# Performance work log

Measured on AMD Instinct MI355X. Metric: run time of the kernel, lower is better.

## Reference

```python
import jax, jax.numpy as jnp
import numpy as np

N = 50000      # nodes
E = 600000     # edges (avg degree 12)
DIN, DE, DH = 17, 1, 128
L, H, C = 3, 4, 32   # layers, heads, per-head channels (DH = H*C)
NEG_SLOPE = 0.2


def setup_inputs() -> dict:
    key = jax.random.key(0)
    ks = jax.random.split(key, 18)
    rn = lambda k, s, sc: jax.random.normal(k, s, jnp.float32) * sc
    return {
        "x": rn(ks[0], (N, DIN), 1.0),
        "edge_index": jax.random.randint(ks[1], (2, E), 0, N, dtype=jnp.int64),
        "edge_attr": rn(ks[2], (E, DE), 1.0),
        "enc_node_w": rn(ks[3], (DIN, DH), 1.0 / np.sqrt(DIN)),
        "enc_node_b": jnp.zeros((DH,), jnp.float32),
        "enc_edge_w": rn(ks[4], (DE, DH), 1.0),
        "enc_edge_b": jnp.zeros((DH,), jnp.float32),
        "lin_w": rn(ks[5], (L, DH, DH), 1.0 / np.sqrt(DH)),
        "lin_edge_w": rn(ks[6], (L, DH, DH), 1.0 / np.sqrt(DH)),
        "att_src": rn(ks[7], (L, H, C), 1.0 / np.sqrt(C)),
        "att_dst": rn(ks[8], (L, H, C), 1.0 / np.sqrt(C)),
        "att_edge": rn(ks[9], (L, H, C), 1.0 / np.sqrt(C)),
        "gat_bias": jnp.zeros((L, DH), jnp.float32),
        "dec_w1": rn(ks[10], (DH, DH), 1.0 / np.sqrt(DH)),
        "dec_b1": jnp.zeros((DH,), jnp.float32),
        "dec_w2": rn(ks[11], (DH, 2), 1.0 / np.sqrt(DH)),
        "dec_b2": jnp.zeros((2,), jnp.float32),
    }


def _gat_layer(x, src, dst, e_attr, W, We, a_src, a_dst, a_edge, bias):
    """PyG GATConv, concat=True, dropout in eval mode (identity).
    x: [N,DH], src/dst: [E2] (self-loops already appended), e_attr: [E2,DH]."""
    n = x.shape[0]
    h = (x @ W).reshape(n, H, C)                       # [N,H,C]
    alpha_src = jnp.einsum('nhc,hc->nh', h, a_src)     # [N,H]
    alpha_dst = jnp.einsum('nhc,hc->nh', h, a_dst)
    e = (e_attr @ We).reshape(-1, H, C)                # [E2,H,C]
    alpha_e = jnp.einsum('ehc,hc->eh', e, a_edge)      # [E2,H]
    logits = jax.nn.leaky_relu(alpha_src[src] + alpha_dst[dst] + alpha_e, NEG_SLOPE)
    # segment softmax over edges grouped by destination node
    mx = jax.ops.segment_max(logits, dst, num_segments=n)          # [N,H]
    num = jnp.exp(logits - mx[dst])                                # [E2,H]
    den = jax.ops.segment_sum(num, dst, num_segments=n)            # [N,H]
    alpha = num / (den[dst] + 1e-16)                               # [E2,H]
    msg = h[src] * alpha[:, :, None]                               # [E2,H,C]
    out = jax.ops.segment_sum(msg, dst, num_segments=n)            # [N,H,C]
    return out.reshape(n, H * C) + bias


def reference(x, edge_index, edge_attr,
              enc_node_w, enc_node_b, enc_edge_w, enc_edge_b,
              lin_w, lin_edge_w, att_src, att_dst, att_edge, gat_bias,
              dec_w1, dec_b1, dec_w2, dec_b2):
    n = x.shape[0]
    src, dst = edge_index[0], edge_index[1]
    h = x @ enc_node_w + enc_node_b                    # node encoder
    ea = edge_attr @ enc_edge_w + enc_edge_b           # edge encoder [E,DH]
    # add_self_loops with fill_value='mean': self-loop attr = mean of incoming edge attrs
    ea_sum = jax.ops.segment_sum(ea, dst, num_segments=n)
    cnt = jax.ops.segment_sum(jnp.ones((ea.shape[0],), ea.dtype), dst, num_segments=n)
    loop_attr = ea_sum / jnp.maximum(cnt, 1.0)[:, None]
    loop_idx = jnp.arange(n, dtype=src.dtype)
    src_f = jnp.concatenate([src, loop_idx])
    dst_f = jnp.concatenate([dst, loop_idx])
    ea_f = jnp.concatenate([ea, loop_attr], axis=0)    # [E+N,DH]
    for l in range(L):
        h = _gat_layer(h, src_f, dst_f, ea_f,
                       lin_w[l], lin_edge_w[l],
                       att_src[l], att_dst[l], att_edge[l], gat_bias[l])
        h = jax.nn.elu(h)
    h = jax.nn.relu(h @ dec_w1 + dec_b1)
    return h @ dec_w2 + dec_b2                          # [N,2]
```

## Files before the change

kernel.cpp:

```cpp
#include <hip/hip_runtime.h>
#include <hip/hip_fp16.h>
#include <math.h>

#define DIN 17
#define DH  128
#define NH  4
#define CC  32
#define NL  3
#define NEG 0.2f

#define PK_SHIFT 44
#define PK_MASK  ((1ULL << PK_SHIFT) - 1)
#define PK_BIAS  16.0f
#define PK_SCALE 1048576.0f

typedef _Float16 hf;
typedef _Float16 f16x8 __attribute__((ext_vector_type(8)));
typedef float    f32x4 __attribute__((ext_vector_type(4)));

#define NT 9

__global__ void pq_kernel(const float* __restrict__ ew, const float* __restrict__ eb,
                          const float* __restrict__ We, const float* __restrict__ ae,
                          float* __restrict__ pq) {
    int lh = blockIdx.x;
    int l = lh >> 2, h = lh & 3;
    int t = threadIdx.x;
    const float* Wel = We + l * DH * DH;
    const float* ael = ae + l * DH + h * CC;
    float p = 0.f, q = 0.f;
    for (int d = t; d < DH; d += 64) {
        const float* row = Wel + d * DH + h * CC;
        float wp = 0.f;
        for (int c = 0; c < CC; ++c) wp += row[c] * ael[c];
        p += ew[d] * wp;
        q += eb[d] * wp;
    }
    for (int o = 32; o > 0; o >>= 1) { p += __shfl_down(p, o, 64); q += __shfl_down(q, o, 64); }
    if (t == 0) { pq[lh * 2 + 0] = p; pq[lh * 2 + 1] = q; }
}

__global__ void vprep(const float* __restrict__ lin_w, const float* __restrict__ att_src,
                      const float* __restrict__ att_dst, float* __restrict__ va) {
    int b = blockIdx.x;
    int l = b >> 3, id = b & 7, hh = id >> 1;
    const float* W = lin_w + (size_t)l * DH * DH;
    const float* a = ((id & 1) ? att_dst : att_src) + l * DH + hh * CC;
    int k = threadIdx.x;
    float s = 0.f;
    #pragma unroll
    for (int c = 0; c < CC; ++c) s += W[k * DH + hh * CC + c] * a[c];
    va[(size_t)b * DH + k] = s;
}

__global__ void wtprep(const float* __restrict__ lin_w, const float* __restrict__ dec_w1,
                       const float* __restrict__ va, hf* __restrict__ wfrag) {
    int b = blockIdx.x;
    int m = b / NT, nt = b % NT;
    int lane = threadIdx.x & 63, kk = threadIdx.x >> 6;
    int colr = lane & 15, kg = lane >> 4;
    hf* dst = wfrag + ((((size_t)b * 4 + kk) * 64) + lane) * 8;
    if (nt < 8) {
        const float* src = (m < 3) ? (lin_w + (size_t)m * DH * DH) : dec_w1;
        #pragma unroll
        for (int jj = 0; jj < 8; ++jj) {
            int k = kk * 32 + kg * 8 + jj;
            dst[jj] = (hf)src[k * DH + nt * 16 + colr];
        }
    } else {
        #pragma unroll
        for (int jj = 0; jj < 8; ++jj) {
            int k = kk * 32 + kg * 8 + jj;
            dst[jj] = (m < 3 && colr < 8) ? (hf)va[((size_t)m * 8 + colr) * DH + k] : (hf)0.f;
        }
    }
}

__global__ void enc_kernel(const float* __restrict__ x, const float* __restrict__ W,
                           const float* __restrict__ b, float* __restrict__ h, int N) {
    __shared__ float wl[DIN][DH];
    __shared__ float xs[32][DIN];
    int tid = threadIdx.x;
    int row0 = blockIdx.x * 32;
    for (int i = tid; i < DIN * DH; i += 256) wl[i / DH][i % DH] = W[i];
    for (int i = tid; i < 32 * DIN; i += 256) {
        int r = i / DIN, k = i % DIN;
        int rr = row0 + r; if (rr > N - 1) rr = N - 1;
        xs[r][k] = x[(size_t)rr * DIN + k];
    }
    __syncthreads();
    int c = tid & 127;
    int g = tid >> 7;
    float bias = b[c];
    #pragma unroll
    for (int r = 0; r < 16; ++r) {
        int row = row0 + g * 16 + r;
        if (row >= N) break;
        float acc = bias;
        #pragma unroll
        for (int k = 0; k < DIN; ++k) acc += xs[g * 16 + r][k] * wl[k][c];
        h[(size_t)row * DH + c] = acc;
    }
}

#define STAGE_ROWS(hsrc)                                                          \
    {                                                                             \
        _Pragma("unroll")                                                         \
        for (int i = 0; i < 4; ++i) {                                             \
            int idx = tid + i * 256;           \
            int r = idx >> 4, ch = idx & 15;                                      \
            int gr = row0 + r; if (gr > N - 1) gr = N - 1;                        \
            const float4* sp = (const float4*)((hsrc) + (size_t)gr * DH + ch * 8);\
            float4 v0 = sp[0], v1 = sp[1];                                        \
            union { uint4 u; hf hx[8]; } pkd;                                     \
            pkd.hx[0] = (hf)v0.x; pkd.hx[1] = (hf)v0.y;                           \
            pkd.hx[2] = (hf)v0.z; pkd.hx[3] = (hf)v0.w;                           \
            pkd.hx[4] = (hf)v1.x; pkd.hx[5] = (hf)v1.y;                           \
            pkd.hx[6] = (hf)v1.z; pkd.hx[7] = (hf)v1.w;                           \
            lds[r * 16 + (ch ^ (r & 7))] = pkd.u;                                 \
        }                                                                         \
        __syncthreads();                                                          \
    }

__global__ void __launch_bounds__(256) layer_node(
        const float* __restrict__ h, const hf* __restrict__ wfrag,
        __half* __restrict__ h1h, float* __restrict__ as_, float* __restrict__ ad_,
        int N) {
    __shared__ uint4 lds[64 * 16];
    int tid = threadIdx.x;
    int row0 = blockIdx.x * 64;
    STAGE_ROWS(h);

    int w = tid >> 6, lane = tid & 63;
    int colr = lane & 15, kg = lane >> 4;
    int lrow = w * 16 + colr;

    f16x8 afr[4];
    #pragma unroll
    for (int kk = 0; kk < 4; ++kk) {
        int ch = (kk * 4 + kg) ^ (colr & 7);
        afr[kk] = *(const f16x8*)&lds[lrow * 16 + ch];
    }

    f32x4 acc[NT];
    #pragma unroll
    for (int nt = 0; nt < NT; ++nt) acc[nt] = (f32x4){0.f, 0.f, 0.f, 0.f};

    const f16x8* wf = (const f16x8*)wfrag;
    #pragma unroll
    for (int nt = 0; nt < NT; ++nt) {
        #pragma unroll
        for (int kk = 0; kk < 4; ++kk) {
            f16x8 bfr = wf[(size_t)(nt * 4 + kk) * 64 + lane];
            acc[nt] = __builtin_amdgcn_mfma_f32_16x16x32_f16(afr[kk], bfr, acc[nt], 0, 0, 0);
        }
    }

    #pragma unroll
    for (int r = 0; r < 4; ++r) {
        int grow = row0 + w * 16 + kg * 4 + r;
        if (grow < N) {
            #pragma unroll
            for (int nt = 0; nt < 8; ++nt)
                h1h[(size_t)grow * DH + nt * 16 + colr] = (__half)(float)acc[nt][r];
        }
    }
    if (colr < 8) {
        int id = colr, hh = id >> 1;
        #pragma unroll
        for (int r = 0; r < 4; ++r) {
            int grow = row0 + w * 16 + kg * 4 + r;
            if (grow < N) {
                float v = (float)acc[8][r];
                if (id & 1) ad_[grow * NH + hh] = v;
                else        as_[grow * NH + hh] = v;
            }
        }
    }
}

__global__ void rank_kernel(const int* __restrict__ ei, const float* __restrict__ ea,
                            unsigned long long* __restrict__ pk, int* __restrict__ rank,
                            int E) {
    int e = blockIdx.x * 256 + threadIdx.x;
    if (e >= E) return;
    int d = ei[E + e];
    unsigned long long enc = (1ULL << PK_SHIFT) |
        (unsigned long long)(int)((ea[e] + PK_BIAS) * PK_SCALE);
    unsigned long long old = atomicAdd(&pk[d], enc);
    rank[e] = (int)(old >> PK_SHIFT);
}

__global__ void scan1(const unsigned long long* __restrict__ pk, int* __restrict__ offs,
                      int* __restrict__ bsum, int N) {
    __shared__ int buf[1024];
    int b = blockIdx.x, t = threadIdx.x, i = b * 1024 + t;
    int v = (i < N) ? (int)(pk[i] >> PK_SHIFT) : 0;
    buf[t] = v;
    __syncthreads();
    int val = v;
    for (int o = 1; o < 1024; o <<= 1) {
        int add = (t >= o) ? buf[t - o] : 0;
        __syncthreads();
        val += add;
        buf[t] = val;
        __syncthreads();
    }
    if (i < N) offs[i] = val - v;
    if (t == 1023) bsum[b] = val;
}

__global__ void scan2(const int* __restrict__ bsum, int* __restrict__ boff, int nb) {
    if (threadIdx.x == 0) {
        int s = 0;
        for (int b = 0; b < nb; ++b) { boff[b] = s; s += bsum[b]; }
    }
}

__global__ void scan3(int* __restrict__ offs, const int* __restrict__ boff,
                      const unsigned long long* __restrict__ pk,
                      int* __restrict__ deg, float* __restrict__ asum, int N) {
    int i = blockIdx.x * 1024 + threadIdx.x;
    if (i >= N) return;
    offs[i] += boff[blockIdx.x];
    unsigned long long p = pk[i];
    int cnt = (int)(p >> PK_SHIFT);
    float s = (float)(p & PK_MASK) * (1.0f / PK_SCALE) - (float)cnt * PK_BIAS;
    deg[i] = cnt;
    asum[i] = s;
}

__global__ void scatter_kernel(const int* __restrict__ ei, const float* __restrict__ ea,
                               const int* __restrict__ offs, const int* __restrict__ rank,
                               int2* __restrict__ csr, int E) {
    int e = blockIdx.x * 256 + threadIdx.x;
    if (e >= E) return;
    int d = ei[E + e];
    int pos = offs[d] + rank[e];
    int2 p; p.x = ei[e]; p.y = __float_as_int(ea[e]);
    csr[pos] = p;
}

__global__ void __launch_bounds__(256) agg_kernel(
        const __half* __restrict__ h1h, const float* __restrict__ as_,
        const float* __restrict__ ad_, const int* __restrict__ offs,
        const int* __restrict__ deg, const float* __restrict__ asum,
        const int2* __restrict__ csr,
        const float* __restrict__ pql, const float* __restrict__ bias,
        float* __restrict__ hout, int N) {
    int n = blockIdx.x * 4 + (threadIdx.x >> 6);
    if (n >= N) return;
    int lane = threadIdx.x & 63;
    int hd = lane >> 4;
    int c0 = lane * 2;
    int off = offs[n], dg = deg[n];
    float adn = ad_[n * NH + hd];
    float pa = pql[hd * 2 + 0], qa = pql[hd * 2 + 1];

    const __half2* h1v = (const __half2*)h1h;

    float sa = asum[n] / fmaxf((float)dg, 1.f);
    float ael = (dg > 0) ? (sa * pa + qa) : 0.f;
    float l0 = as_[n * NH + hd] + adn + ael;
    l0 = fmaxf(l0, NEG * l0);

    float2 hv = __half22float2(h1v[(size_t)n * 64 + lane]);
    float numS = __expf(l0);
    float denA = numS, a0A = numS * hv.x, a1A = numS * hv.y;
    float denB = 0.f,  a0B = 0.f,         a1B = 0.f;

    int i = 0;
    for (; i + 4 <= dg; i += 4) {
        int2 e0 = csr[off + i + 0];
        int2 e1 = csr[off + i + 1];
        int2 e2 = csr[off + i + 2];
        int2 e3 = csr[off + i + 3];
        __half2 q0 = h1v[(size_t)e0.x * 64 + lane];
        __half2 q1 = h1v[(size_t)e1.x * 64 + lane];
        __half2 q2 = h1v[(size_t)e2.x * 64 + lane];
        __half2 q3 = h1v[(size_t)e3.x * 64 + lane];
        float s0 = as_[e0.x * NH + hd];
        float s1 = as_[e1.x * NH + hd];
        float s2 = as_[e2.x * NH + hd];
        float s3 = as_[e3.x * NH + hd];
        float t0 = s0 + adn + __int_as_float(e0.y) * pa + qa;
        float t1 = s1 + adn + __int_as_float(e1.y) * pa + qa;
        float t2 = s2 + adn + __int_as_float(e2.y) * pa + qa;
        float t3 = s3 + adn + __int_as_float(e3.y) * pa + qa;
        t0 = fmaxf(t0, NEG * t0);
        t1 = fmaxf(t1, NEG * t1);
        t2 = fmaxf(t2, NEG * t2);
        t3 = fmaxf(t3, NEG * t3);
        float n0 = __expf(t0);
        float n1 = __expf(t1);
        float n2 = __expf(t2);
        float n3 = __expf(t3);
        float2 g0 = __half22float2(q0);
        float2 g1 = __half22float2(q1);
        float2 g2 = __half22float2(q2);
        float2 g3 = __half22float2(q3);
        denA += n0 + n2; denB += n1 + n3;
        a0A = fmaf(n0, g0.x, a0A); a0B = fmaf(n1, g1.x, a0B);
        a0A = fmaf(n2, g2.x, a0A); a0B = fmaf(n3, g3.x, a0B);
        a1A = fmaf(n0, g0.y, a1A); a1B = fmaf(n1, g1.y, a1B);
        a1A = fmaf(n2, g2.y, a1A); a1B = fmaf(n3, g3.y, a1B);
    }
    for (; i < dg; ++i) {
        int2 ep = csr[off + i];
        __half2 qs = h1v[(size_t)ep.x * 64 + lane];
        float lg = as_[ep.x * NH + hd] + adn + __int_as_float(ep.y) * pa + qa;
        lg = fmaxf(lg, NEG * lg);
        float num = __expf(lg);
        float2 gs = __half22float2(qs);
        denA += num;
        a0A = fmaf(num, gs.x, a0A);
        a1A = fmaf(num, gs.y, a1A);
    }
    float den = denA + denB;
    float a0 = a0A + a0B, a1 = a1A + a1B;
    float inv = 1.f / (den + 1e-16f);
    float o0 = a0 * inv + bias[c0];
    float o1 = a1 * inv + bias[c0 + 1];
    o0 = (o0 > 0.f) ? o0 : expm1f(o0);
    o1 = (o1 > 0.f) ? o1 : expm1f(o1);
    hout[(size_t)n * DH + c0] = o0;
    hout[(size_t)n * DH + c0 + 1] = o1;
}

__global__ void __launch_bounds__(256) dec_kernel(
        const float* __restrict__ h, const hf* __restrict__ wfrag,
        const float* __restrict__ b1, const float* __restrict__ w2,
        const float* __restrict__ b2, float* __restrict__ out, int N) {
    __shared__ uint4 lds[64 * 16];
    int tid = threadIdx.x;
    int row0 = blockIdx.x * 64;
    STAGE_ROWS(h);

    int w = tid >> 6, lane = tid & 63;
    int colr = lane & 15, kg = lane >> 4;
    int lrow = w * 16 + colr;

    f16x8 afr[4];
    #pragma unroll
    for (int kk = 0; kk < 4; ++kk) {
        int ch = (kk * 4 + kg) ^ (colr & 7);
        afr[kk] = *(const f16x8*)&lds[lrow * 16 + ch];
    }

    f32x4 acc[8];
    #pragma unroll
    for (int nt = 0; nt < 8; ++nt) acc[nt] = (f32x4){0.f, 0.f, 0.f, 0.f};

    const f16x8* wf = (const f16x8*)wfrag;
    #pragma unroll
    for (int nt = 0; nt < 8; ++nt) {
        #pragma unroll
        for (int kk = 0; kk < 4; ++kk) {
            f16x8 bfr = wf[(size_t)(nt * 4 + kk) * 64 + lane];
            acc[nt] = __builtin_amdgcn_mfma_f32_16x16x32_f16(afr[kk], bfr, acc[nt], 0, 0, 0);
        }
    }

    float bb0 = b2[0], bb1 = b2[1];
    float b1v[8], w20[8], w21[8];
    #pragma unroll
    for (int nt = 0; nt < 8; ++nt) {
        int col = nt * 16 + colr;
        b1v[nt] = b1[col];
        w20[nt] = w2[col * 2 + 0];
        w21[nt] = w2[col * 2 + 1];
    }
    #pragma unroll
    for (int r = 0; r < 4; ++r) {
        float p0 = 0.f, p1 = 0.f;
        #pragma unroll
        for (int nt = 0; nt < 8; ++nt) {
            float hid = fmaxf((float)acc[nt][r] + b1v[nt], 0.f);
            p0 = fmaf(hid, w20[nt], p0);
            p1 = fmaf(hid, w21[nt], p1);
        }
        #pragma unroll
        for (int o = 1; o < 16; o <<= 1) {
            p0 += __shfl_xor(p0, o, 16);
            p1 += __shfl_xor(p1, o, 16);
        }
        int grow = row0 + w * 16 + kg * 4 + r;
        if (colr == 0 && grow < N) {
            out[grow * 2 + 0] = p0 + bb0;
            out[grow * 2 + 1] = p1 + bb1;
        }
    }
}

extern "C" void kernel_launch(void* const* d_in, const int* in_sizes, int n_in,
                              void* d_out, int out_size, void* d_ws, size_t ws_size,
                              hipStream_t stream) {
    const float* x          = (const float*)d_in[0];
    const int*   ei         = (const int*)d_in[1];
    const float* eattr      = (const float*)d_in[2];
    const float* enc_node_w = (const float*)d_in[3];
    const float* enc_node_b = (const float*)d_in[4];
    const float* enc_edge_w = (const float*)d_in[5];
    const float* enc_edge_b = (const float*)d_in[6];
    const float* lin_w      = (const float*)d_in[7];
    const float* lin_edge_w = (const float*)d_in[8];
    const float* att_src    = (const float*)d_in[9];
    const float* att_dst    = (const float*)d_in[10];
    const float* att_edge   = (const float*)d_in[11];
    const float* gat_bias   = (const float*)d_in[12];
    const float* dec_w1     = (const float*)d_in[13];
    const float* dec_b1     = (const float*)d_in[14];
    const float* dec_w2     = (const float*)d_in[15];
    const float* dec_b2     = (const float*)d_in[16];

    const int E = in_sizes[2];
    const int N = in_sizes[0] / DIN;

    char* w = (char*)d_ws;
    auto alloc = [&](size_t bytes) -> void* {
        void* p = (void*)w;
        w += (bytes + 511) & ~((size_t)511);
        return p;
    };
    float*  h     = (float*)alloc((size_t)N * DH * 4);
    __half* h1h   = (__half*)alloc((size_t)N * DH * 2);
    float* as_    = (float*)alloc((size_t)N * NH * 4);
    float* ad_    = (float*)alloc((size_t)N * NH * 4);
    unsigned long long* pk = (unsigned long long*)alloc((size_t)N * 8);
    int*   rank   = (int*)alloc((size_t)E * 4);
    int*   deg    = (int*)alloc((size_t)N * 4);
    float* asum   = (float*)alloc((size_t)N * 4);
    int*   offs   = (int*)alloc((size_t)N * 4);
    int*   bsum   = (int*)alloc(64 * 4);
    int*   boff   = (int*)alloc(64 * 4);
    int2*  csr    = (int2*)alloc((size_t)E * 8);
    float* pq     = (float*)alloc(NL * NH * 2 * 4);
    float* va     = (float*)alloc((size_t)NL * 8 * DH * 4);
    hf*    wfrag  = (hf*)alloc((size_t)4 * NT * 4 * 64 * 8 * 2);

    hipMemsetAsync(pk, 0, (size_t)N * 8, stream);

    pq_kernel<<<NL * NH, 64, 0, stream>>>(enc_edge_w, enc_edge_b, lin_edge_w, att_edge, pq);
    vprep<<<NL * 8, DH, 0, stream>>>(lin_w, att_src, att_dst, va);
    wtprep<<<4 * NT, 256, 0, stream>>>(lin_w, dec_w1, va, wfrag);
    enc_kernel<<<(N + 31) / 32, 256, 0, stream>>>(x, enc_node_w, enc_node_b, h, N);
    rank_kernel<<<(E + 255) / 256, 256, 0, stream>>>(ei, eattr, pk, rank, E);

    int nb = (N + 1023) / 1024;
    scan1<<<nb, 1024, 0, stream>>>(pk, offs, bsum, N);
    scan2<<<1, 64, 0, stream>>>(bsum, boff, nb);
    scan3<<<nb, 1024, 0, stream>>>(offs, boff, pk, deg, asum, N);
    scatter_kernel<<<(E + 255) / 256, 256, 0, stream>>>(ei, eattr, offs, rank, csr, E);

    const size_t mstride = (size_t)NT * 4 * 64 * 8;
    for (int l = 0; l < NL; ++l) {
        layer_node<<<(N + 63) / 64, 256, 0, stream>>>(h, wfrag + (size_t)l * mstride,
                                                      h1h, as_, ad_, N);
        agg_kernel<<<(N + 3) / 4, 256, 0, stream>>>(h1h, as_, ad_, offs, deg, asum, csr,
                                                    pq + l * NH * 2, gat_bias + l * DH, h, N);
    }
    dec_kernel<<<(N + 63) / 64, 256, 0, stream>>>(h, wfrag + (size_t)3 * mstride,
                                                  dec_b1, dec_w2, dec_b2,
                                                  (float*)d_out, N);
}
```

Measured before the change: 328.4 us.

## Store node features in fp16, fuse prep and scan kernels, unroll aggregation by 8

The inter-layer node feature buffer changes from fp32 to fp16, which halves its write traffic in the encoder and aggregation kernels and its read traffic in the GEMM staging. The fp32-to-fp16 conversion moves from the GEMM staging step to the producers. The vprep kernel is folded into wtprep and scan2 into scan3, which removes two tiny launches. The aggregation gather loop gains an 8-edge unrolled stage for more memory-level parallelism. The fp16 storage costs nothing extra because the GEMM already cast its input to fp16, so numerics stay essentially unchanged.

```diff
diff --git a/kernel.cpp b/kernel.cpp
--- a/kernel.cpp
+++ b/kernel.cpp
@@ -40,21 +40,9 @@
     if (t == 0) { pq[lh * 2 + 0] = p; pq[lh * 2 + 1] = q; }
 }
 
-__global__ void vprep(const float* __restrict__ lin_w, const float* __restrict__ att_src,
-                      const float* __restrict__ att_dst, float* __restrict__ va) {
-    int b = blockIdx.x;
-    int l = b >> 3, id = b & 7, hh = id >> 1;
-    const float* W = lin_w + (size_t)l * DH * DH;
-    const float* a = ((id & 1) ? att_dst : att_src) + l * DH + hh * CC;
-    int k = threadIdx.x;
-    float s = 0.f;
-    #pragma unroll
-    for (int c = 0; c < CC; ++c) s += W[k * DH + hh * CC + c] * a[c];
-    va[(size_t)b * DH + k] = s;
-}
-
 __global__ void wtprep(const float* __restrict__ lin_w, const float* __restrict__ dec_w1,
-                       const float* __restrict__ va, hf* __restrict__ wfrag) {
+                       const float* __restrict__ att_src, const float* __restrict__ att_dst,
+                       hf* __restrict__ wfrag) {
     int b = blockIdx.x;
     int m = b / NT, nt = b % NT;
     int lane = threadIdx.x & 63, kk = threadIdx.x >> 6;
@@ -67,17 +55,26 @@
             int k = kk * 32 + kg * 8 + jj;
             dst[jj] = (hf)src[k * DH + nt * 16 + colr];
         }
-    } else {
+    } else if (m < 3 && colr < 8) {
+        int hh = colr >> 1;
+        const float* W = lin_w + (size_t)m * DH * DH;
+        const float* a = ((colr & 1) ? att_dst : att_src) + m * DH + hh * CC;
         #pragma unroll
         for (int jj = 0; jj < 8; ++jj) {
             int k = kk * 32 + kg * 8 + jj;
-            dst[jj] = (m < 3 && colr < 8) ? (hf)va[((size_t)m * 8 + colr) * DH + k] : (hf)0.f;
-        }
+            float s = 0.f;
+            #pragma unroll
+            for (int c = 0; c < CC; ++c) s += W[k * DH + hh * CC + c] * a[c];
+            dst[jj] = (hf)s;
+        }
+    } else {
+        #pragma unroll
+        for (int jj = 0; jj < 8; ++jj) dst[jj] = (hf)0.f;
     }
 }
 
 __global__ void enc_kernel(const float* __restrict__ x, const float* __restrict__ W,
-                           const float* __restrict__ b, float* __restrict__ h, int N) {
+                           const float* __restrict__ b, hf* __restrict__ h16, int N) {
     __shared__ float wl[DIN][DH];
     __shared__ float xs[32][DIN];
     int tid = threadIdx.x;
@@ -99,37 +96,31 @@
         float acc = bias;
         #pragma unroll
         for (int k = 0; k < DIN; ++k) acc += xs[g * 16 + r][k] * wl[k][c];
-        h[(size_t)row * DH + c] = acc;
-    }
-}
-
-#define STAGE_ROWS(hsrc)                                                          \
+        h16[(size_t)row * DH + c] = (hf)acc;
+    }
+}
+
+#define STAGE_ROWS16(hsrc)                                                        \
     {                                                                             \
         _Pragma("unroll")                                                         \
         for (int i = 0; i < 4; ++i) {                                             \
             int idx = tid + i * 256;           \
             int r = idx >> 4, ch = idx & 15;                                      \
             int gr = row0 + r; if (gr > N - 1) gr = N - 1;                        \
-            const float4* sp = (const float4*)((hsrc) + (size_t)gr * DH + ch * 8);\
-            float4 v0 = sp[0], v1 = sp[1];                                        \
-            union { uint4 u; hf hx[8]; } pkd;                                     \
-            pkd.hx[0] = (hf)v0.x; pkd.hx[1] = (hf)v0.y;                           \
-            pkd.hx[2] = (hf)v0.z; pkd.hx[3] = (hf)v0.w;                           \
-            pkd.hx[4] = (hf)v1.x; pkd.hx[5] = (hf)v1.y;                           \
-            pkd.hx[6] = (hf)v1.z; pkd.hx[7] = (hf)v1.w;                           \
-            lds[r * 16 + (ch ^ (r & 7))] = pkd.u;                                 \
+            lds[r * 16 + (ch ^ (r & 7))] =                                        \
+                ((const uint4*)((hsrc) + (size_t)gr * DH))[ch];                   \
         }                                                                         \
         __syncthreads();                                                          \
     }
 
 __global__ void __launch_bounds__(256) layer_node(
-        const float* __restrict__ h, const hf* __restrict__ wfrag,
+        const hf* __restrict__ h16, const hf* __restrict__ wfrag,
         __half* __restrict__ h1h, float* __restrict__ as_, float* __restrict__ ad_,
         int N) {
     __shared__ uint4 lds[64 * 16];
     int tid = threadIdx.x;
     int row0 = blockIdx.x * 64;
-    STAGE_ROWS(h);
+    STAGE_ROWS16(h16);
 
     int w = tid >> 6, lane = tid & 63;
     int colr = lane & 15, kg = lane >> 4;
@@ -210,19 +201,19 @@
     if (t == 1023) bsum[b] = val;
 }
 
-__global__ void scan2(const int* __restrict__ bsum, int* __restrict__ boff, int nb) {
+__global__ void scan3(int* __restrict__ offs, const int* __restrict__ bsum,
+                      const unsigned long long* __restrict__ pk,
+                      int* __restrict__ deg, float* __restrict__ asum, int N) {
+    __shared__ int base;
     if (threadIdx.x == 0) {
         int s = 0;
-        for (int b = 0; b < nb; ++b) { boff[b] = s; s += bsum[b]; }
-    }
-}
-
-__global__ void scan3(int* __restrict__ offs, const int* __restrict__ boff,
-                      const unsigned long long* __restrict__ pk,
-                      int* __restrict__ deg, float* __restrict__ asum, int N) {
+        for (int b = 0; b < (int)blockIdx.x; ++b) s += bsum[b];
+        base = s;
+    }
+    __syncthreads();
     int i = blockIdx.x * 1024 + threadIdx.x;
     if (i >= N) return;
-    offs[i] += boff[blockIdx.x];
+    offs[i] += base;
     unsigned long long p = pk[i];
     int cnt = (int)(p >> PK_SHIFT);
     float s = (float)(p & PK_MASK) * (1.0f / PK_SCALE) - (float)cnt * PK_BIAS;
@@ -247,7 +238,7 @@
         const int* __restrict__ deg, const float* __restrict__ asum,
         const int2* __restrict__ csr,
         const float* __restrict__ pql, const float* __restrict__ bias,
-        float* __restrict__ hout, int N) {
+        hf* __restrict__ hout, int N) {
     int n = blockIdx.x * 4 + (threadIdx.x >> 6);
     if (n >= N) return;
     int lane = threadIdx.x & 63;
@@ -270,40 +261,45 @@
     float denB = 0.f,  a0B = 0.f,         a1B = 0.f;
 
     int i = 0;
+    for (; i + 8 <= dg; i += 8) {
+        int2 e[8];
+        #pragma unroll
+        for (int j = 0; j < 8; ++j) e[j] = csr[off + i + j];
+        __half2 q[8];
+        #pragma unroll
+        for (int j = 0; j < 8; ++j) q[j] = h1v[(size_t)e[j].x * 64 + lane];
+        float s[8];
+        #pragma unroll
+        for (int j = 0; j < 8; ++j) s[j] = as_[e[j].x * NH + hd];
+        #pragma unroll
+        for (int j = 0; j < 8; ++j) {
+            float t = s[j] + adn + __int_as_float(e[j].y) * pa + qa;
+            t = fmaxf(t, NEG * t);
+            float nm = __expf(t);
+            float2 g = __half22float2(q[j]);
+            if (j & 1) { denB += nm; a0B = fmaf(nm, g.x, a0B); a1B = fmaf(nm, g.y, a1B); }
+            else       { denA += nm; a0A = fmaf(nm, g.x, a0A); a1A = fmaf(nm, g.y, a1A); }
+        }
+    }
     for (; i + 4 <= dg; i += 4) {
-        int2 e0 = csr[off + i + 0];
-        int2 e1 = csr[off + i + 1];
-        int2 e2 = csr[off + i + 2];
-        int2 e3 = csr[off + i + 3];
-        __half2 q0 = h1v[(size_t)e0.x * 64 + lane];
-        __half2 q1 = h1v[(size_t)e1.x * 64 + lane];
-        __half2 q2 = h1v[(size_t)e2.x * 64 + lane];
-        __half2 q3 = h1v[(size_t)e3.x * 64 + lane];
-        float s0 = as_[e0.x * NH + hd];
-        float s1 = as_[e1.x * NH + hd];
-        float s2 = as_[e2.x * NH + hd];
-        float s3 = as_[e3.x * NH + hd];
-        float t0 = s0 + adn + __int_as_float(e0.y) * pa + qa;
-        float t1 = s1 + adn + __int_as_float(e1.y) * pa + qa;
-        float t2 = s2 + adn + __int_as_float(e2.y) * pa + qa;
-        float t3 = s3 + adn + __int_as_float(e3.y) * pa + qa;
-        t0 = fmaxf(t0, NEG * t0);
-        t1 = fmaxf(t1, NEG * t1);
-        t2 = fmaxf(t2, NEG * t2);
-        t3 = fmaxf(t3, NEG * t3);
-        float n0 = __expf(t0);
-        float n1 = __expf(t1);
-        float n2 = __expf(t2);
-        float n3 = __expf(t3);
-        float2 g0 = __half22float2(q0);
-        float2 g1 = __half22float2(q1);
-        float2 g2 = __half22float2(q2);
-        float2 g3 = __half22float2(q3);
-        denA += n0 + n2; denB += n1 + n3;
-        a0A = fmaf(n0, g0.x, a0A); a0B = fmaf(n1, g1.x, a0B);
-        a0A = fmaf(n2, g2.x, a0A); a0B = fmaf(n3, g3.x, a0B);
-        a1A = fmaf(n0, g0.y, a1A); a1B = fmaf(n1, g1.y, a1B);
-        a1A = fmaf(n2, g2.y, a1A); a1B = fmaf(n3, g3.y, a1B);
+        int2 e[4];
+        #pragma unroll
+        for (int j = 0; j < 4; ++j) e[j] = csr[off + i + j];
+        __half2 q[4];
+        #pragma unroll
+        for (int j = 0; j < 4; ++j) q[j] = h1v[(size_t)e[j].x * 64 + lane];
+        float s[4];
+        #pragma unroll
+        for (int j = 0; j < 4; ++j) s[j] = as_[e[j].x * NH + hd];
+        #pragma unroll
+        for (int j = 0; j < 4; ++j) {
+            float t = s[j] + adn + __int_as_float(e[j].y) * pa + qa;
+            t = fmaxf(t, NEG * t);
+            float nm = __expf(t);
+            float2 g = __half22float2(q[j]);
+            if (j & 1) { denB += nm; a0B = fmaf(nm, g.x, a0B); a1B = fmaf(nm, g.y, a1B); }
+            else       { denA += nm; a0A = fmaf(nm, g.x, a0A); a1A = fmaf(nm, g.y, a1A); }
+        }
     }
     for (; i < dg; ++i) {
         int2 ep = csr[off + i];
@@ -323,18 +319,19 @@
     float o1 = a1 * inv + bias[c0 + 1];
     o0 = (o0 > 0.f) ? o0 : expm1f(o0);
     o1 = (o1 > 0.f) ? o1 : expm1f(o1);
-    hout[(size_t)n * DH + c0] = o0;
-    hout[(size_t)n * DH + c0 + 1] = o1;
+    union { unsigned int u; hf hx[2]; } st;
+    st.hx[0] = (hf)o0; st.hx[1] = (hf)o1;
+    ((unsigned int*)hout)[(size_t)n * 64 + lane] = st.u;
 }
 
 __global__ void __launch_bounds__(256) dec_kernel(
-        const float* __restrict__ h, const hf* __restrict__ wfrag,
+        const hf* __restrict__ h16, const hf* __restrict__ wfrag,
         const float* __restrict__ b1, const float* __restrict__ w2,
         const float* __restrict__ b2, float* __restrict__ out, int N) {
     __shared__ uint4 lds[64 * 16];
     int tid = threadIdx.x;
     int row0 = blockIdx.x * 64;
-    STAGE_ROWS(h);
+    STAGE_ROWS16(h16);
 
     int w = tid >> 6, lane = tid & 63;
     int colr = lane & 15, kg = lane >> 4;
@@ -422,7 +419,7 @@
         w += (bytes + 511) & ~((size_t)511);
         return p;
     };
-    float*  h     = (float*)alloc((size_t)N * DH * 4);
+    hf*     h16   = (hf*)alloc((size_t)N * DH * 2);
     __half* h1h   = (__half*)alloc((size_t)N * DH * 2);
     float* as_    = (float*)alloc((size_t)N * NH * 4);
     float* ad_    = (float*)alloc((size_t)N * NH * 4);
@@ -432,34 +429,30 @@
     float* asum   = (float*)alloc((size_t)N * 4);
     int*   offs   = (int*)alloc((size_t)N * 4);
     int*   bsum   = (int*)alloc(64 * 4);
-    int*   boff   = (int*)alloc(64 * 4);
     int2*  csr    = (int2*)alloc((size_t)E * 8);
     float* pq     = (float*)alloc(NL * NH * 2 * 4);
-    float* va     = (float*)alloc((size_t)NL * 8 * DH * 4);
     hf*    wfrag  = (hf*)alloc((size_t)4 * NT * 4 * 64 * 8 * 2);
 
     hipMemsetAsync(pk, 0, (size_t)N * 8, stream);
 
     pq_kernel<<<NL * NH, 64, 0, stream>>>(enc_edge_w, enc_edge_b, lin_edge_w, att_edge, pq);
-    vprep<<<NL * 8, DH, 0, stream>>>(lin_w, att_src, att_dst, va);
-    wtprep<<<4 * NT, 256, 0, stream>>>(lin_w, dec_w1, va, wfrag);
-    enc_kernel<<<(N + 31) / 32, 256, 0, stream>>>(x, enc_node_w, enc_node_b, h, N);
+    wtprep<<<4 * NT, 256, 0, stream>>>(lin_w, dec_w1, att_src, att_dst, wfrag);
+    enc_kernel<<<(N + 31) / 32, 256, 0, stream>>>(x, enc_node_w, enc_node_b, h16, N);
     rank_kernel<<<(E + 255) / 256, 256, 0, stream>>>(ei, eattr, pk, rank, E);
 
     int nb = (N + 1023) / 1024;
     scan1<<<nb, 1024, 0, stream>>>(pk, offs, bsum, N);
-    scan2<<<1, 64, 0, stream>>>(bsum, boff, nb);
-    scan3<<<nb, 1024, 0, stream>>>(offs, boff, pk, deg, asum, N);
+    scan3<<<nb, 1024, 0, stream>>>(offs, bsum, pk, deg, asum, N);
     scatter_kernel<<<(E + 255) / 256, 256, 0, stream>>>(ei, eattr, offs, rank, csr, E);
 
     const size_t mstride = (size_t)NT * 4 * 64 * 8;
     for (int l = 0; l < NL; ++l) {
-        layer_node<<<(N + 63) / 64, 256, 0, stream>>>(h, wfrag + (size_t)l * mstride,
+        layer_node<<<(N + 63) / 64, 256, 0, stream>>>(h16, wfrag + (size_t)l * mstride,
                                                       h1h, as_, ad_, N);
         agg_kernel<<<(N + 3) / 4, 256, 0, stream>>>(h1h, as_, ad_, offs, deg, asum, csr,
-                                                    pq + l * NH * 2, gat_bias + l * DH, h, N);
-    }
-    dec_kernel<<<(N + 63) / 64, 256, 0, stream>>>(h, wfrag + (size_t)3 * mstride,
+                                                    pq + l * NH * 2, gat_bias + l * DH, h16, N);
+    }
+    dec_kernel<<<(N + 63) / 64, 256, 0, stream>>>(h16, wfrag + (size_t)3 * mstride,
                                                   dec_b1, dec_w2, dec_b2,
                                                   (float*)d_out, N);
 }
```

Measured after the change: 327.0 us. About the same (-0.4%).
